# Performance work log

Measured on AMD Instinct MI355X. Metric: run time of the kernel, lower is better.

The kernel has to match this reference:

```python
import jax, jax.numpy as jnp
import numpy as np

B, L, F, H, O = 128, 2048, 128, 256, 128
NT = 5  # tickersteps


def setup_inputs() -> dict:
    key = jax.random.key(0)
    ks = jax.random.split(key, 10)
    x = jax.random.normal(ks[0], (B, L, F), dtype=jnp.float32)
    true_seq_lens = jax.random.randint(ks[1], (B,), 1, L + 1)
    s = 0.05
    W = jax.random.normal(ks[2], (F, 3 * H), dtype=jnp.float32) * s   # fwd weights [ci|ig|og]
    R = jax.random.normal(ks[3], (H, 3 * H), dtype=jnp.float32) * s   # recurrent weights [ci|ig|og]
    # biases: b_ci=0, b_ig ~ N(-5,1), b_og=0  (forget gate has no weights/bias -> fg = 1)
    b_ig = jax.random.normal(ks[4], (H,), dtype=jnp.float32) - 5.0
    b = jnp.concatenate([jnp.zeros(H, jnp.float32), b_ig, jnp.zeros(H, jnp.float32)])
    b_ticker = jax.random.normal(ks[5], (3 * H,), dtype=jnp.float32) * s  # tickerstep biases
    Wp = jax.random.normal(ks[6], (H, H), dtype=jnp.float32) * s
    bp = jnp.zeros((H,), jnp.float32)
    Wo = jax.random.normal(ks[7], (O, H), dtype=jnp.float32) * s
    bo = jnp.zeros((O,), jnp.float32)
    return {"x": x, "true_seq_lens": true_seq_lens, "W": W, "R": R, "b": b,
            "b_ticker": b_ticker, "Wp": Wp, "bp": bp, "Wo": Wo, "bo": bo}


def _lstm_final_h(x, true_seq_lens, W, R, b, b_ticker):
    Bv, Lv, _ = x.shape
    Hv = R.shape[0]
    T = Lv + NT
    xp = jnp.pad(x, ((0, 0), (0, NT), (0, 0)))            # zero input during tickersteps
    xs = jnp.swapaxes(xp, 0, 1)                            # [T, B, F]
    ts = jnp.arange(T)
    lens = true_seq_lens.astype(jnp.int32)

    def step(carry, inp):
        h, c = carry
        x_t, t = inp
        in_seq = t < lens                                  # [B]
        in_tick = (t >= lens) & (t < lens + NT)
        active = in_seq | in_tick
        x_t = jnp.where(in_seq[:, None], x_t, 0.0)
        pre = x_t @ W + h @ R + b + jnp.where(in_tick[:, None], b_ticker, 0.0)  # [B, 3H]
        ci = jnp.tanh(pre[:, :Hv])
        ig = jax.nn.sigmoid(pre[:, Hv:2 * Hv])
        og = jax.nn.sigmoid(pre[:, 2 * Hv:])
        c_new = c + ci * ig                                # forget gate disabled -> fg = 1
        h_new = jnp.tanh(c_new) * og
        m = active[:, None]
        return (jnp.where(m, h_new, h), jnp.where(m, c_new, c)), None

    h0 = jnp.zeros((Bv, Hv), x.dtype)
    c0 = jnp.zeros((Bv, Hv), x.dtype)
    (h, _), _ = jax.lax.scan(step, (h0, c0), (xs, ts))
    return h


def reference(x, true_seq_lens, W, R, b, b_ticker, Wp, bp, Wo, bo):
    h = _lstm_final_h(x, true_seq_lens, W, R, b, b_ticker)   # [B, H] final state after tickersteps
    h = h @ Wp.T + bp                                        # pre_fc_out
    return h @ Wo.T + bo                                     # fc_out
```

## Files before the change

### kernel.cpp

```cpp
#include <hip/hip_runtime.h>

#define BB    128
#define LL    2048
#define FF    128
#define HH    256
#define OO    128
#define NTICK 5
#define GC    16
#define NCG   8
#define CH    4
#define DRING 128
#define NPS   8
#define NPL   16
#define MAXT  (LL + NTICK)
#define MAXCH ((MAXT + CH - 1) / CH)
#define RDY8  0x0101010101010101ULL

typedef __attribute__((ext_vector_type(8))) _Float16 half8;
typedef __attribute__((ext_vector_type(4))) float f32x4;

union U64H8 { unsigned long long u[2]; _Float16 h[8]; };
union U64H4 { unsigned long long u; _Float16 h[4]; };

__device__ __forceinline__ float fast_rcp(float x) { return __builtin_amdgcn_rcpf(x); }

__device__ __forceinline__ unsigned long long sysload_u64(const unsigned long long* p) {
  return __hip_atomic_load(p, __ATOMIC_RELAXED, __HIP_MEMORY_SCOPE_SYSTEM);
}
__device__ __forceinline__ void sysstore_u64(unsigned long long* p, unsigned long long v) {
  __hip_atomic_store(p, v, __ATOMIC_RELAXED, __HIP_MEMORY_SCOPE_SYSTEM);
}
__device__ __forceinline__ int sysload_i32(const int* p) {
  return __hip_atomic_load(p, __ATOMIC_RELAXED, __HIP_MEMORY_SCOPE_SYSTEM);
}
__device__ __forceinline__ void sysstore_i32(int* p, int v) {
  __hip_atomic_store(p, v, __ATOMIC_RELAXED, __HIP_MEMORY_SCOPE_SYSTEM);
}
__device__ __forceinline__ void sysstore_u8(unsigned char* p, unsigned char v) {
  __hip_atomic_store(p, v, __ATOMIC_RELAXED, __HIP_MEMORY_SCOPE_SYSTEM);
}

extern "C" __global__ __launch_bounds__(512, 1)
void lstm_all(const float* __restrict__ x, const int* __restrict__ lens,
              const float* __restrict__ W, const float* __restrict__ R,
              const float* __restrict__ bvec, const float* __restrict__ btk,
              unsigned long long* ring, unsigned char* readyb,
              int* prog, float* __restrict__ h_final)
{
  const int tid  = threadIdx.x;
  const int lane = tid & 63;
  const int wv   = tid >> 6;
  const int quad = lane >> 4;
  const int nl   = lane & 15;
  const int bx   = blockIdx.x;

  __shared__ int lens_s[BB];
  if (tid < BB) lens_s[tid] = lens[tid];
  __syncthreads();

  if (bx < NCG) {
    const int cg = bx, cbase = cg * GC;
    __shared__ float    pre_s[GC][772];
    __shared__ float    c_s[GC][260];
    __shared__ _Float16 h_s[GC][264];

    for (int i = tid; i < GC * 772; i += 512) ((float*)pre_s)[i] = 0.f;
    for (int i = tid; i < GC * 260; i += 512) ((float*)c_s)[i] = 0.f;
    for (int i = tid; i < GC * 264; i += 512) ((_Float16*)h_s)[i] = (_Float16)0.f;

    int mxl = 0;
    #pragma unroll
    for (int i = 0; i < GC; i++) mxl = max(mxl, lens_s[cbase + i]);
    const int Tg = mxl + NTICK;

    half8 rfr[6][8];
    const int colw = wv * 96;
    #pragma unroll
    for (int tile = 0; tile < 6; tile++) {
      const int col = colw + tile * 16 + nl;
      #pragma unroll
      for (int kc = 0; kc < 8; kc++) {
        const int k0 = kc * 32 + quad * 8;
        half8 v;
        #pragma unroll
        for (int j = 0; j < 8; j++) v[j] = (_Float16)R[(k0 + j) * (3 * HH) + col];
        rfr[tile][kc] = v;
      }
    }

    const int m  = tid >> 5;
    const int hj = (tid & 31) * 8;
    const int lenm = lens_s[cbase + m];

    const unsigned long long* rb = (const unsigned long long*)readyb;

    while (sysload_u64(rb + 0) != RDY8) {}
    asm volatile("" ::: "memory");
    unsigned long long xw[6];
    {
      const unsigned long long* rp = ring + ((((long)0 * BB + cbase + m) * 768 + hj) >> 2);
      xw[0] = sysload_u64(rp);       xw[1] = sysload_u64(rp + 1);
      xw[2] = sysload_u64(rp + 64);  xw[3] = sysload_u64(rp + 65);
      xw[4] = sysload_u64(rp + 128); xw[5] = sysload_u64(rp + 129);
    }
    unsigned long long rvn = sysload_u64(rb + 1);
    int cur_chunk = 0;
    __syncthreads();

    for (int t = 0; t < Tg; ++t) {
      if (t > 0) {
        f32x4 acc[6];
        #pragma unroll
        for (int i = 0; i < 6; i++) acc[i] = (f32x4){0.f, 0.f, 0.f, 0.f};
        const _Float16* hrow = &h_s[nl][0];
        #pragma unroll
        for (int kc = 0; kc < 8; kc++) {
          const half8 a = *(const half8*)(hrow + kc * 32 + quad * 8);
          #pragma unroll
          for (int tile = 0; tile < 6; tile++)
            acc[tile] = __builtin_amdgcn_mfma_f32_16x16x32_f16(rfr[tile][kc], a, acc[tile], 0, 0, 0);
        }
        #pragma unroll
        for (int tile = 0; tile < 6; tile++)
          *(f32x4*)(&pre_s[nl][colw + tile * 16 + quad * 4]) = acc[tile];
      }
      __syncthreads();

      if (t < lenm + NTICK) {
        U64H8 uc, ui, uo;
        uc.u[0] = xw[0]; uc.u[1] = xw[1];
        ui.u[0] = xw[2]; ui.u[1] = xw[3];
        uo.u[0] = xw[4]; uo.u[1] = xw[5];
        const float* pr = &pre_s[m][0];
        float pci[8], pig[8], pog[8], cc[8], hh[8];
        *(float4*)(pci)     = *(const float4*)(pr + hj);
        *(float4*)(pci + 4) = *(const float4*)(pr + hj + 4);
        *(float4*)(pig)     = *(const float4*)(pr + 256 + hj);
        *(float4*)(pig + 4) = *(const float4*)(pr + 256 + hj + 4);
        *(float4*)(pog)     = *(const float4*)(pr + 512 + hj);
        *(float4*)(pog + 4) = *(const float4*)(pr + 512 + hj + 4);
        *(float4*)(cc)      = *(const float4*)(&c_s[m][hj]);
        *(float4*)(cc + 4)  = *(const float4*)(&c_s[m][hj + 4]);
        #pragma unroll
        for (int d = 0; d < 8; d++) {
          const float pc = pci[d] + (float)uc.h[d];
          const float pi = pig[d] + (float)ui.h[d];
          const float po = pog[d] + (float)uo.h[d];
          const float ea = __expf(2.f * __builtin_fminf(pc, 15.f));
          const float eb = __expf(-pi);
          const float cn = cc[d] + (ea - 1.f) * fast_rcp((ea + 1.f) * (1.f + eb));
          const float ec = __expf(2.f * __builtin_fminf(cn, 15.f));
          const float ed = __expf(-po);
          hh[d] = (ec - 1.f) * fast_rcp((ec + 1.f) * (1.f + ed));
          cc[d] = cn;
        }
        *(float4*)(&c_s[m][hj])     = *(float4*)(cc);
        *(float4*)(&c_s[m][hj + 4]) = *(float4*)(cc + 4);
        _Float16 hp8[8];
        #pragma unroll
        for (int d = 0; d < 8; d++) hp8[d] = (_Float16)hh[d];
        *(half8*)(&h_s[m][hj]) = *(half8*)hp8;
        if (t == lenm + NTICK - 1) {
          float* hf = h_final + (cbase + m) * HH + hj;
          *(float4*)(hf)     = *(float4*)(hh);
          *(float4*)(hf + 4) = *(float4*)(hh + 4);
        }
      }

      if (t + 1 < Tg) {
        const int nc = (t + 1) >> 2;
        if (nc != cur_chunk) {
          while (rvn != RDY8) rvn = sysload_u64(rb + nc);
          cur_chunk = nc;
          rvn = (nc + 1 < MAXCH) ? sysload_u64(rb + nc + 1) : RDY8;
        }
        asm volatile("" ::: "memory");
        const int slot = (t + 1) & (DRING - 1);
        const unsigned long long* rp = ring + ((((long)slot * BB + cbase + m) * 768 + hj) >> 2);
        xw[0] = sysload_u64(rp);       xw[1] = sysload_u64(rp + 1);
        xw[2] = sysload_u64(rp + 64);  xw[3] = sysload_u64(rp + 65);
        xw[4] = sysload_u64(rp + 128); xw[5] = sysload_u64(rp + 129);
      }
      __syncthreads();
      if (tid == 0) sysstore_i32(prog + cg, t);
    }
    if (tid == 0) sysstore_i32(prog + cg, 1 << 20);

  } else {
    const int pid = bx - NCG;
    const int s   = pid & 7;
    const int pl  = pid >> 3;

    int mxall = 0;
    #pragma unroll 8
    for (int i = 0; i < BB; i++) mxall = max(mxall, lens_s[i]);
    const int Tall = mxall + NTICK;
    const int nch  = (Tall + CH - 1) / CH;

    half8 wfr[4];
    float bias4[4], tick4[4];
    int col0w = 0;
    if (wv < 6) {
      col0w = s * 96 + wv * 16;
      #pragma unroll
      for (int kc = 0; kc < 4; kc++) {
        const int k0 = kc * 32 + quad * 8;
        half8 v;
        #pragma unroll
        for (int j = 0; j < 8; j++) v[j] = (_Float16)W[(k0 + j) * (3 * HH) + col0w + nl];
        wfr[kc] = v;
      }
      *(float4*)bias4 = *(const float4*)(bvec + col0w + quad * 4);
      *(float4*)tick4 = *(const float4*)(btk  + col0w + quad * 4);
    }

    for (int c = pl; c < nch; c += NPL) {
      if (c * CH >= DRING) {
        if (tid == 0) {
          const int need = c * CH + CH - DRING;
          for (;;) {
            int mn = 0x7fffffff;
            #pragma unroll
            for (int g = 0; g < NCG; g++) mn = min(mn, sysload_i32(prog + g));
            if (mn >= need) break;
          }
        }
        __syncthreads();
      }
      if (wv < 6) {
        for (int tt = 0; tt < CH; tt++) {
          const int t = c * CH + tt;
          const int slot = t & (DRING - 1);
          #pragma unroll 2
          for (int bt = 0; bt < 8; bt++) {
            const int b = bt * 16 + nl;
            const int lenb = lens_s[b];
            f32x4 acc = {0.f, 0.f, 0.f, 0.f};
            if (t < LL) {
              const float* xp = x + ((long)b * LL + t) * FF + quad * 8;
              #pragma unroll
              for (int kc = 0; kc < 4; kc++) {
                const float4 u0 = *(const float4*)(xp + kc * 32);
                const float4 u1 = *(const float4*)(xp + kc * 32 + 4);
                half8 a;
                a[0] = (_Float16)u0.x; a[1] = (_Float16)u0.y;
                a[2] = (_Float16)u0.z; a[3] = (_Float16)u0.w;
                a[4] = (_Float16)u1.x; a[5] = (_Float16)u1.y;
                a[6] = (_Float16)u1.z; a[7] = (_Float16)u1.w;
                acc = __builtin_amdgcn_mfma_f32_16x16x32_f16(wfr[kc], a, acc, 0, 0, 0);
              }
            }
            U64H4 pk;
            const bool in_x  = (t < lenb);
            const bool in_tk = (t >= lenb) && (t < lenb + NTICK);
            #pragma unroll
            for (int r = 0; r < 4; r++) {
              float v = bias4[r];
              if (in_x)  v += acc[r];
              if (in_tk) v += tick4[r];
              pk.h[r] = (_Float16)v;
            }
            sysstore_u64(ring + ((((long)slot * BB + b) * 768 + col0w + quad * 4) >> 2), pk.u);
          }
        }
      }
      __syncthreads();
      if (tid == 0) sysstore_u8(readyb + c * 8 + s, (unsigned char)1);
    }
  }
}

extern "C" __global__ void proj_hp(const float* __restrict__ h,
                                   const float* __restrict__ Wp,
                                   const float* __restrict__ bp,
                                   float* __restrict__ hp)
{
  const int bb = blockIdx.x;
  const int j  = threadIdx.x;
  const float4* hv = (const float4*)(h + bb * HH);
  const float4* wr = (const float4*)(Wp + j * HH);
  float s = 0.f;
  for (int k = 0; k < HH / 4; k++) {
    const float4 a = hv[k], w = wr[k];
    s += a.x * w.x + a.y * w.y + a.z * w.z + a.w * w.w;
  }
  hp[bb * HH + j] = s + bp[j];
}

extern "C" __global__ void proj_out(const float* __restrict__ hp,
                                    const float* __restrict__ Wo,
                                    const float* __restrict__ bo,
                                    float* __restrict__ out)
{
  const int bb = blockIdx.x;
  const int o  = threadIdx.x;
  const float4* hv = (const float4*)(hp + bb * HH);
  const float4* wr = (const float4*)(Wo + o * HH);
  float s = 0.f;
  for (int k = 0; k < HH / 4; k++) {
    const float4 a = hv[k], w = wr[k];
    s += a.x * w.x + a.y * w.y + a.z * w.z + a.w * w.w;
  }
  out[bb * OO + o] = s + bo[o];
}

extern "C" void kernel_launch(void* const* d_in, const int* in_sizes, int n_in,
                              void* d_out, int out_size, void* d_ws, size_t ws_size,
                              hipStream_t stream)
{
  const float* x    = (const float*)d_in[0];
  const int*   ln   = (const int*)  d_in[1];
  const float* W    = (const float*)d_in[2];
  const float* R    = (const float*)d_in[3];
  const float* bvec = (const float*)d_in[4];
  const float* btk  = (const float*)d_in[5];
  const float* Wp   = (const float*)d_in[6];
  const float* bp   = (const float*)d_in[7];
  const float* Wo   = (const float*)d_in[8];
  const float* bo   = (const float*)d_in[9];
  float* out = (float*)d_out;

  char* ws = (char*)d_ws;
  int*                prog    = (int*)ws;
  unsigned char*      readyb  = (unsigned char*)(ws + 64);
  float*              h_final = (float*)(ws + 8192);
  float*              hp      = (float*)(ws + 8192 + 131072);
  unsigned long long* ring    = (unsigned long long*)(ws + (1 << 20));

  hipLaunchKernelGGL(lstm_all, dim3(NCG + NPS * NPL), dim3(512), 0, stream,
                     x, ln, W, R, bvec, btk, ring, readyb, prog, h_final);
  hipLaunchKernelGGL(proj_hp,  dim3(BB), dim3(HH), 0, stream, h_final, Wp, bp, hp);
  hipLaunchKernelGGL(proj_out, dim3(BB), dim3(OO), 0, stream, hp, Wo, bo, out);
}
```

Measured before the change: 6.043 ms.

## Fuse gate math into MFMA accumulators and double-buffer h in LDS

New measurement: 7.166 ms. 18.6% more time.

```diff
diff --git a/kernel.cpp b/kernel.cpp
--- a/kernel.cpp
+++ b/kernel.cpp
@@ -19,7 +19,6 @@
 typedef __attribute__((ext_vector_type(8))) _Float16 half8;
 typedef __attribute__((ext_vector_type(4))) float f32x4;
 
-union U64H8 { unsigned long long u[2]; _Float16 h[8]; };
 union U64H4 { unsigned long long u; _Float16 h[4]; };
 
 __device__ __forceinline__ float fast_rcp(float x) { return __builtin_amdgcn_rcpf(x); }
@@ -38,6 +37,12 @@
 }
 __device__ __forceinline__ void sysstore_u8(unsigned char* p, unsigned char v) {
   __hip_atomic_store(p, v, __ATOMIC_RELAXED, __HIP_MEMORY_SCOPE_SYSTEM);
+}
+
+__device__ __forceinline__ void sync_lds_only() {
+  asm volatile("s_waitcnt lgkmcnt(0)" ::: "memory");
+  __builtin_amdgcn_s_barrier();
+  asm volatile("" ::: "memory");
 }
 
 extern "C" __global__ __launch_bounds__(512, 1)
@@ -60,13 +65,9 @@
 
   if (bx < NCG) {
     const int cg = bx, cbase = cg * GC;
-    __shared__ float    pre_s[GC][772];
-    __shared__ float    c_s[GC][260];
-    __shared__ _Float16 h_s[GC][264];
-
-    for (int i = tid; i < GC * 772; i += 512) ((float*)pre_s)[i] = 0.f;
-    for (int i = tid; i < GC * 260; i += 512) ((float*)c_s)[i] = 0.f;
-    for (int i = tid; i < GC * 264; i += 512) ((_Float16*)h_s)[i] = (_Float16)0.f;
+    __shared__ _Float16 h_s[2][GC][264];
+
+    for (int i = tid; i < 2 * GC * 264; i += 512) ((_Float16*)h_s)[i] = (_Float16)0.f;
 
     int mxl = 0;
     #pragma unroll
@@ -74,98 +75,48 @@
     const int Tg = mxl + NTICK;
 
     half8 rfr[6][8];
-    const int colw = wv * 96;
     #pragma unroll
-    for (int tile = 0; tile < 6; tile++) {
-      const int col = colw + tile * 16 + nl;
-      #pragma unroll
-      for (int kc = 0; kc < 8; kc++) {
-        const int k0 = kc * 32 + quad * 8;
-        half8 v;
-        #pragma unroll
-        for (int j = 0; j < 8; j++) v[j] = (_Float16)R[(k0 + j) * (3 * HH) + col];
-        rfr[tile][kc] = v;
+    for (int g = 0; g < 3; g++) {
+      #pragma unroll
+      for (int tl = 0; tl < 2; tl++) {
+        const int col = g * 256 + wv * 32 + tl * 16 + nl;
+        #pragma unroll
+        for (int kc = 0; kc < 8; kc++) {
+          const int k0 = kc * 32 + quad * 8;
+          half8 v;
+          #pragma unroll
+          for (int j = 0; j < 8; j++) v[j] = (_Float16)R[(k0 + j) * (3 * HH) + col];
+          rfr[g * 2 + tl][kc] = v;
+        }
       }
     }
 
-    const int m  = tid >> 5;
-    const int hj = (tid & 31) * 8;
-    const int lenm = lens_s[cbase + m];
+    const int b    = cbase + nl;
+    const int lenN = lens_s[b];
+    const int cb   = wv * 8 + quad;
+
+    float cst[8], hst[8];
+    #pragma unroll
+    for (int d = 0; d < 8; d++) { cst[d] = 0.f; hst[d] = 0.f; }
 
     const unsigned long long* rb = (const unsigned long long*)readyb;
 
     while (sysload_u64(rb + 0) != RDY8) {}
     asm volatile("" ::: "memory");
     unsigned long long xw[6];
-    {
-      const unsigned long long* rp = ring + ((((long)0 * BB + cbase + m) * 768 + hj) >> 2);
-      xw[0] = sysload_u64(rp);       xw[1] = sysload_u64(rp + 1);
-      xw[2] = sysload_u64(rp + 64);  xw[3] = sysload_u64(rp + 65);
-      xw[4] = sysload_u64(rp + 128); xw[5] = sysload_u64(rp + 129);
-    }
+    #pragma unroll
+    for (int g = 0; g < 3; g++)
+      #pragma unroll
+      for (int tl = 0; tl < 2; tl++)
+        xw[g * 2 + tl] = sysload_u64(ring + (g * 64 + tl * 4 + cb) * 128 + b);
     unsigned long long rvn = sysload_u64(rb + 1);
     int cur_chunk = 0;
     __syncthreads();
 
     for (int t = 0; t < Tg; ++t) {
-      if (t > 0) {
-        f32x4 acc[6];
-        #pragma unroll
-        for (int i = 0; i < 6; i++) acc[i] = (f32x4){0.f, 0.f, 0.f, 0.f};
-        const _Float16* hrow = &h_s[nl][0];
-        #pragma unroll
-        for (int kc = 0; kc < 8; kc++) {
-          const half8 a = *(const half8*)(hrow + kc * 32 + quad * 8);
-          #pragma unroll
-          for (int tile = 0; tile < 6; tile++)
-            acc[tile] = __builtin_amdgcn_mfma_f32_16x16x32_f16(rfr[tile][kc], a, acc[tile], 0, 0, 0);
-        }
-        #pragma unroll
-        for (int tile = 0; tile < 6; tile++)
-          *(f32x4*)(&pre_s[nl][colw + tile * 16 + quad * 4]) = acc[tile];
-      }
-      __syncthreads();
-
-      if (t < lenm + NTICK) {
-        U64H8 uc, ui, uo;
-        uc.u[0] = xw[0]; uc.u[1] = xw[1];
-        ui.u[0] = xw[2]; ui.u[1] = xw[3];
-        uo.u[0] = xw[4]; uo.u[1] = xw[5];
-        const float* pr = &pre_s[m][0];
-        float pci[8], pig[8], pog[8], cc[8], hh[8];
-        *(float4*)(pci)     = *(const float4*)(pr + hj);
-        *(float4*)(pci + 4) = *(const float4*)(pr + hj + 4);
-        *(float4*)(pig)     = *(const float4*)(pr + 256 + hj);
-        *(float4*)(pig + 4) = *(const float4*)(pr + 256 + hj + 4);
-        *(float4*)(pog)     = *(const float4*)(pr + 512 + hj);
-        *(float4*)(pog + 4) = *(const float4*)(pr + 512 + hj + 4);
-        *(float4*)(cc)      = *(const float4*)(&c_s[m][hj]);
-        *(float4*)(cc + 4)  = *(const float4*)(&c_s[m][hj + 4]);
-        #pragma unroll
-        for (int d = 0; d < 8; d++) {
-          const float pc = pci[d] + (float)uc.h[d];
-          const float pi = pig[d] + (float)ui.h[d];
-          const float po = pog[d] + (float)uo.h[d];
-          const float ea = __expf(2.f * __builtin_fminf(pc, 15.f));
-          const float eb = __expf(-pi);
-          const float cn = cc[d] + (ea - 1.f) * fast_rcp((ea + 1.f) * (1.f + eb));
-          const float ec = __expf(2.f * __builtin_fminf(cn, 15.f));
-          const float ed = __expf(-po);
-          hh[d] = (ec - 1.f) * fast_rcp((ec + 1.f) * (1.f + ed));
-          cc[d] = cn;
-        }
-        *(float4*)(&c_s[m][hj])     = *(float4*)(cc);
-        *(float4*)(&c_s[m][hj + 4]) = *(float4*)(cc + 4);
-        _Float16 hp8[8];
-        #pragma unroll
-        for (int d = 0; d < 8; d++) hp8[d] = (_Float16)hh[d];
-        *(half8*)(&h_s[m][hj]) = *(half8*)hp8;
-        if (t == lenm + NTICK - 1) {
-          float* hf = h_final + (cbase + m) * HH + hj;
-          *(float4*)(hf)     = *(float4*)(hh);
-          *(float4*)(hf + 4) = *(float4*)(hh + 4);
-        }
-      }
+      U64H4 u[6];
+      #pragma unroll
+      for (int i = 0; i < 6; i++) u[i].u = xw[i];
 
       if (t + 1 < Tg) {
         const int nc = (t + 1) >> 2;
@@ -176,12 +127,69 @@
         }
         asm volatile("" ::: "memory");
         const int slot = (t + 1) & (DRING - 1);
-        const unsigned long long* rp = ring + ((((long)slot * BB + cbase + m) * 768 + hj) >> 2);
-        xw[0] = sysload_u64(rp);       xw[1] = sysload_u64(rp + 1);
-        xw[2] = sysload_u64(rp + 64);  xw[3] = sysload_u64(rp + 65);
-        xw[4] = sysload_u64(rp + 128); xw[5] = sysload_u64(rp + 129);
-      }
-      __syncthreads();
+        const unsigned long long* rp = ring + (long)slot * (192 * 128);
+        #pragma unroll
+        for (int g = 0; g < 3; g++)
+          #pragma unroll
+          for (int tl = 0; tl < 2; tl++)
+            xw[g * 2 + tl] = sysload_u64(rp + (g * 64 + tl * 4 + cb) * 128 + b);
+      }
+
+      f32x4 acc[6];
+      #pragma unroll
+      for (int i = 0; i < 6; i++) acc[i] = (f32x4){0.f, 0.f, 0.f, 0.f};
+      if (t > 0) {
+        const _Float16* hrow = &h_s[t & 1][nl][0];
+        #pragma unroll
+        for (int kc = 0; kc < 8; kc++) {
+          const half8 a = *(const half8*)(hrow + kc * 32 + quad * 8);
+          #pragma unroll
+          for (int i = 0; i < 6; i++)
+            acc[i] = __builtin_amdgcn_mfma_f32_16x16x32_f16(rfr[i][kc], a, acc[i], 0, 0, 0);
+        }
+      }
+
+      if (t < lenN + NTICK) {
+        #pragma unroll
+        for (int tl = 0; tl < 2; tl++) {
+          #pragma unroll
+          for (int r = 0; r < 4; r++) {
+            const int d = tl * 4 + r;
+            const float pc = acc[tl][r]     + (float)u[tl].h[r];
+            const float pi = acc[2 + tl][r] + (float)u[2 + tl].h[r];
+            const float po = acc[4 + tl][r] + (float)u[4 + tl].h[r];
+            const float ea = __expf(2.f * __builtin_fminf(pc, 15.f));
+            const float eb = __expf(-pi);
+            const float cn = cst[d] + (ea - 1.f) * fast_rcp((ea + 1.f) * (1.f + eb));
+            const float ec = __expf(2.f * __builtin_fminf(cn, 15.f));
+            const float ed = __expf(-po);
+            hst[d] = (ec - 1.f) * fast_rcp((ec + 1.f) * (1.f + ed));
+            cst[d] = cn;
+          }
+        }
+        if (t == lenN + NTICK - 1) {
+          float* hf = h_final + b * HH + wv * 32 + quad * 4;
+          float4 v0, v1;
+          v0.x = hst[0]; v0.y = hst[1]; v0.z = hst[2]; v0.w = hst[3];
+          v1.x = hst[4]; v1.y = hst[5]; v1.z = hst[6]; v1.w = hst[7];
+          *(float4*)(hf)      = v0;
+          *(float4*)(hf + 16) = v1;
+        }
+      }
+
+      {
+        U64H4 p0, p1;
+        #pragma unroll
+        for (int r = 0; r < 4; r++) {
+          p0.h[r] = (_Float16)hst[r];
+          p1.h[r] = (_Float16)hst[4 + r];
+        }
+        _Float16* hw = &h_s[(t + 1) & 1][nl][wv * 32 + quad * 4];
+        *(unsigned long long*)(hw)      = p0.u;
+        *(unsigned long long*)(hw + 16) = p1.u;
+      }
+
+      sync_lds_only();
       if (tid == 0) sysstore_i32(prog + cg, t);
     }
     if (tid == 0) sysstore_i32(prog + cg, 1 << 20);
@@ -199,9 +207,10 @@
 
     half8 wfr[4];
     float bias4[4], tick4[4];
-    int col0w = 0;
+    int c4b = 0;
     if (wv < 6) {
-      col0w = s * 96 + wv * 16;
+      const int col0w = s * 96 + wv * 16;
+      c4b = (s * 24 + wv * 4 + quad) * 128;
       #pragma unroll
       for (int kc = 0; kc < 4; kc++) {
         const int k0 = kc * 32 + quad * 8;
@@ -231,13 +240,14 @@
         for (int tt = 0; tt < CH; tt++) {
           const int t = c * CH + tt;
           const int slot = t & (DRING - 1);
+          unsigned long long* sp = ring + (long)slot * (192 * 128) + c4b;
           #pragma unroll 2
           for (int bt = 0; bt < 8; bt++) {
-            const int b = bt * 16 + nl;
-            const int lenb = lens_s[b];
+            const int bb = bt * 16 + nl;
+            const int lenb = lens_s[bb];
             f32x4 acc = {0.f, 0.f, 0.f, 0.f};
             if (t < LL) {
-              const float* xp = x + ((long)b * LL + t) * FF + quad * 8;
+              const float* xp = x + ((long)bb * LL + t) * FF + quad * 8;
               #pragma unroll
               for (int kc = 0; kc < 4; kc++) {
                 const float4 u0 = *(const float4*)(xp + kc * 32);
@@ -260,7 +270,7 @@
               if (in_tk) v += tick4[r];
               pk.h[r] = (_Float16)v;
             }
-            sysstore_u64(ring + ((((long)slot * BB + b) * 768 + col0w + quad * 4) >> 2), pk.u);
+            sysstore_u64(sp + bb, pk.u);
           }
         }
       }
```
